# Optimization experiments

Measured on AMD Instinct MI355X. Metric: run time of the kernel, lower is better.

Reference implementation:

```python
import jax, jax.numpy as jnp
import numpy as np

NEG_BIG = -9e15

def mish(x):
    return x * jnp.tanh(jax.nn.softplus(x))

def setup_inputs() -> dict:
    key = jax.random.key(0)
    k1, k2, k3, k4 = jax.random.split(key, 4)
    N, Fin, Fout = 8192, 512, 256
    x = jax.random.normal(k1, (N, Fin), dtype=jnp.float32)
    adj = jax.random.randint(k2, (N, N), 0, 2, dtype=jnp.int32)
    # xavier-uniform-like params
    wlim = np.sqrt(6.0 / (Fin + Fout)).astype(np.float32)
    weight = jax.random.uniform(k3, (Fin, Fout), dtype=jnp.float32, minval=-wlim, maxval=wlim)
    alim = np.sqrt(6.0 / (2 * Fout + 1)).astype(np.float32)
    a = jax.random.uniform(k4, (2 * Fout, 1), dtype=jnp.float32, minval=-alim, maxval=alim)
    return {"x": x, "adj": adj, "weight": weight, "a": a}

def reference(x, adj, weight, a):
    Fout = weight.shape[1]
    h = x @ weight                      # [N, Fout]
    # e[i,j] = mish(h_i . a1 + h_j . a2) -- avoids O(N^2 * 2F) a_input
    s_src = h @ a[:Fout, 0]             # [N]
    s_dst = h @ a[Fout:, 0]             # [N]
    e = mish(s_src[:, None] + s_dst[None, :])  # [N, N]
    logits = jnp.where(adj > 0, e, NEG_BIG)
    attention = jax.nn.softmax(logits, axis=1)  # dropout skipped (eval mode)
    h_prime = attention @ h             # [N, Fout]
    return mish(h_prime)
```

## Files before the change

kernel.cpp:

```cpp
#include <hip/hip_runtime.h>
#include <hip/hip_fp16.h>

#define NROWS 8192
#define FIN   512
#define FOUT  256

using f16   = _Float16;
using f16x8 = __attribute__((ext_vector_type(8))) f16;
using f16x4 = __attribute__((ext_vector_type(4))) f16;
using f32x4 = __attribute__((ext_vector_type(4))) float;
using i32x4 = __attribute__((ext_vector_type(4))) int;

#define MFMA16(a, b, c) __builtin_amdgcn_mfma_f32_16x16x32_f16((a), (b), (c), 0, 0, 0)

__device__ __forceinline__ float mish_f(float x) {
  float t = __expf(x);
  float u = t * (t + 2.0f);
  return x * (u / (u + 2.0f));
}

__device__ __forceinline__ float dot4(float4 p, float4 q) {
  return p.x * q.x + p.y * q.y + p.z * q.z + p.w * q.w;
}

__global__ __launch_bounds__(256) void k0_prep_w(
    const float* __restrict__ wgt, const float* __restrict__ a,
    f16* __restrict__ wB_hi, f16* __restrict__ wB_lo,
    float* __restrict__ wa1, float* __restrict__ wa2) {
  int k = blockIdx.x * 256 + threadIdx.x;
  if (k >= FIN) return;
  int kt = k >> 5, g2 = (k >> 3) & 3, e = k & 7;
  float acc1 = 0.f, acc2 = 0.f;
  for (int f = 0; f < FOUT; ++f) {
    float v = wgt[(size_t)k * FOUT + f];
    acc1 += v * a[f];
    acc2 += v * a[FOUT + f];
    f16 h = (f16)v;
    size_t base = (((size_t)(kt * 16 + (f >> 4)) * 64) + g2 * 16 + (f & 15)) * 8 + e;
    wB_hi[base] = h;
    wB_lo[base] = (f16)(v - (float)h);
  }
  wa1[k] = acc1;
  wa2[k] = acc2;
}

__global__ __launch_bounds__(256) void k2_scores(
    const float* __restrict__ x, const float* __restrict__ wa1,
    const float* __restrict__ wa2, float* __restrict__ s_src,
    float* __restrict__ s_dst, unsigned int* __restrict__ maxd_enc) {
  int wv = threadIdx.x >> 6, lane = threadIdx.x & 63;
  int row = blockIdx.x * 4 + wv;
  const float4* xr = (const float4*)(x + (size_t)row * FIN);
  float4 x0 = xr[lane * 2], x1 = xr[lane * 2 + 1];
  const float4* w1 = (const float4*)wa1;
  const float4* w2 = (const float4*)wa2;
  float p1 = dot4(x0, w1[lane * 2]) + dot4(x1, w1[lane * 2 + 1]);
  float p2 = dot4(x0, w2[lane * 2]) + dot4(x1, w2[lane * 2 + 1]);
  for (int off = 32; off > 0; off >>= 1) {
    p1 += __shfl_down(p1, off);
    p2 += __shfl_down(p2, off);
  }
  if (lane == 0) {
    s_src[row] = p1;
    s_dst[row] = p2;
    unsigned b = __float_as_uint(p2);
    unsigned enc = (b & 0x80000000u) ? ~b : (b | 0x80000000u);
    atomicMax(maxd_enc, enc);
  }
}

__global__ __launch_bounds__(256) void k1_gemm_h(
    const float* __restrict__ x, const f16* __restrict__ wB_hi,
    const f16* __restrict__ wB_lo, f16* __restrict__ hB_hi,
    f16* __restrict__ hB_lo) {
  __shared__ float xs[64][36];
  int mt = blockIdx.x >> 1, ns = blockIdx.x & 1;
  int m0 = mt * 64;
  int tid = threadIdx.x;
  int w = tid >> 6, lane = tid & 63;
  int g = lane >> 4, lr = lane & 15;

  f32x4 acc[4][2] = {};

  for (int kk = 0; kk < FIN; kk += 32) {
    {
      int r = tid >> 3;
      int c = (tid & 7) * 4;
      *(float4*)(&xs[r][c])      = *(const float4*)(x + (size_t)(m0 + r) * FIN + kk + c);
      *(float4*)(&xs[r + 32][c]) = *(const float4*)(x + (size_t)(m0 + r + 32) * FIN + kk + c);
    }
    __syncthreads();
    int kt = kk >> 5;
    f16x8 bh[2], bl[2];
#pragma unroll
    for (int ct = 0; ct < 2; ++ct) {
      int ft = ns * 8 + w * 2 + ct;
      size_t slot = ((size_t)(kt * 16 + ft) * 64 + lane) * 8;
      bh[ct] = *(const f16x8*)(wB_hi + slot);
      bl[ct] = *(const f16x8*)(wB_lo + slot);
    }
#pragma unroll
    for (int rt = 0; rt < 4; ++rt) {
      const float* ap = &xs[rt * 16 + lr][g * 8];
      f16x8 ah, al;
#pragma unroll
      for (int e = 0; e < 8; ++e) {
        float v = ap[e];
        f16 h = (f16)v;
        ah[e] = h;
        al[e] = (f16)(v - (float)h);
      }
#pragma unroll
      for (int ct = 0; ct < 2; ++ct) {
        acc[rt][ct] = MFMA16(ah, bh[ct], acc[rt][ct]);
        acc[rt][ct] = MFMA16(ah, bl[ct], acc[rt][ct]);
        acc[rt][ct] = MFMA16(al, bh[ct], acc[rt][ct]);
      }
    }
    __syncthreads();
  }

#pragma unroll
  for (int rt = 0; rt < 4; ++rt) {
    int jg0 = m0 + rt * 16 + g * 4;
    int jt = jg0 >> 5, g2 = (jg0 >> 3) & 3, e0 = jg0 & 7;
#pragma unroll
    for (int ct = 0; ct < 2; ++ct) {
      int f = ns * 128 + w * 32 + ct * 16 + lr;
      size_t base = (((size_t)(jt * 16 + (f >> 4)) * 64) + g2 * 16 + (f & 15)) * 8 + e0;
      f16x4 hv, lv;
#pragma unroll
      for (int rg = 0; rg < 4; ++rg) {
        float v = acc[rt][ct][rg];
        f16 h = (f16)v;
        hv[rg] = h;
        lv[rg] = (f16)(v - (float)h);
      }
      *(f16x4*)(hB_hi + base) = hv;
      *(f16x4*)(hB_lo + base) = lv;
    }
  }
}

__global__ __launch_bounds__(256) void k3_attn(
    const int* __restrict__ adj, const f16* __restrict__ hB_hi,
    const f16* __restrict__ hB_lo, const float* __restrict__ s_src,
    const float* __restrict__ s_dst, const unsigned int* __restrict__ maxd_enc,
    float* __restrict__ num, float* __restrict__ Zbuf) {
  __shared__ float sd_lds[1024];
  __shared__ f16x8 pbuf[2][4][64];

  int it = blockIdx.x >> 3, jc = blockIdx.x & 7;
  int i0 = it * 64;
  int j0 = jc * 1024;
  int tid = threadIdx.x;
  int w = tid >> 6, lane = tid & 63;
  int g = lane >> 4, lr = lane & 15;

  *(float4*)(&sd_lds[tid * 4]) = *(const float4*)(s_dst + j0 + tid * 4);

  unsigned enc = *maxd_enc;
  float maxd = (enc & 0x80000000u) ? __uint_as_float(enc & 0x7fffffffu)
                                   : __uint_as_float(~enc);
  int ip = i0 + w * 16 + lr;
  float s_i = s_src[ip];
  float m_i = fmaxf(0.f, s_i + maxd);
  const int* adjrow = adj + (size_t)ip * NROWS + j0 + g * 8;

  __syncthreads();

  f32x4 acc[4][4] = {};
  f32x4 accz = {};
  f16x8 ones;
#pragma unroll
  for (int e = 0; e < 8; ++e) ones[e] = (f16)1.0f;

  i32x4 adjA = *(const i32x4*)(adjrow);
  i32x4 adjB = *(const i32x4*)(adjrow + 4);

  for (int st = 0; st < 32; ++st) {
    i32x4 nadjA = adjA, nadjB = adjB;
    if (st < 31) {
      nadjA = *(const i32x4*)(adjrow + (st + 1) * 32);
      nadjB = *(const i32x4*)(adjrow + (st + 1) * 32 + 4);
    }
    float4 sd0 = *(const float4*)(&sd_lds[st * 32 + g * 8]);
    float4 sd1 = *(const float4*)(&sd_lds[st * 32 + g * 8 + 4]);
    float sdv[8] = {sd0.x, sd0.y, sd0.z, sd0.w, sd1.x, sd1.y, sd1.z, sd1.w};

    f16x8 pa;
#pragma unroll
    for (int e = 0; e < 8; ++e) {
      float s = s_i + sdv[e];
      float t = __expf(s);
      float u = t * (t + 2.0f);
      float sc = s * (u / (u + 2.0f));
      float p = __expf(sc - m_i);
      int av = (e < 4) ? adjA[e] : adjB[e - 4];
      pa[e] = (av != 0) ? (f16)p : (f16)0.0f;
    }
    pbuf[st & 1][w][lane] = pa;
    accz = MFMA16(pa, ones, accz);
    __syncthreads();

    f16x8 afr[4];
#pragma unroll
    for (int rt = 0; rt < 4; ++rt) afr[rt] = pbuf[st & 1][rt][lane];

    int jt = jc * 32 + st;
#pragma unroll
    for (int ct = 0; ct < 4; ++ct) {
      int ft = w * 4 + ct;
      size_t slot = ((size_t)(jt * 16 + ft) * 64 + lane) * 8;
      f16x8 bhv = *(const f16x8*)(hB_hi + slot);
      f16x8 blv = *(const f16x8*)(hB_lo + slot);
#pragma unroll
      for (int rt = 0; rt < 4; ++rt) {
        acc[rt][ct] = MFMA16(afr[rt], bhv, acc[rt][ct]);
        acc[rt][ct] = MFMA16(afr[rt], blv, acc[rt][ct]);
      }
    }
    adjA = nadjA;
    adjB = nadjB;
  }

#pragma unroll
  for (int rt = 0; rt < 4; ++rt) {
    int ib = i0 + rt * 16 + g * 4;
#pragma unroll
    for (int ct = 0; ct < 4; ++ct) {
      int f = w * 64 + ct * 16 + lr;
#pragma unroll
      for (int rg = 0; rg < 4; ++rg)
        atomicAdd(&num[(size_t)(ib + rg) * FOUT + f], acc[rt][ct][rg]);
    }
  }
  if (lr == 0) {
    int ib = i0 + w * 16 + g * 4;
#pragma unroll
    for (int rg = 0; rg < 4; ++rg)
      atomicAdd(&Zbuf[ib + rg], accz[rg]);
  }
}

__global__ __launch_bounds__(256) void k4_final(float* __restrict__ out,
                                                const float* __restrict__ Zbuf) {
  int idx = blockIdx.x * 256 + threadIdx.x;
  int row = idx >> 6;
  float rz = 1.0f / Zbuf[row];
  float4 v = *(float4*)(out + (size_t)idx * 4);
  v.x = mish_f(v.x * rz);
  v.y = mish_f(v.y * rz);
  v.z = mish_f(v.z * rz);
  v.w = mish_f(v.w * rz);
  *(float4*)(out + (size_t)idx * 4) = v;
}

extern "C" void kernel_launch(void* const* d_in, const int* in_sizes, int n_in,
                              void* d_out, int out_size, void* d_ws, size_t ws_size,
                              hipStream_t stream) {
  const float* x   = (const float*)d_in[0];
  const int*   adj = (const int*)d_in[1];
  const float* wgt = (const float*)d_in[2];
  const float* a   = (const float*)d_in[3];
  float* out = (float*)d_out;

  char* ws = (char*)d_ws;
  f16* hB_hi = (f16*)ws;
  f16* hB_lo = (f16*)(ws + (4u << 20));
  f16* wB_hi = (f16*)(ws + (8u << 20));
  f16* wB_lo = (f16*)(ws + (8u << 20) + (256u << 10));
  float* wa1   = (float*)(ws + (8u << 20) + (512u << 10));
  float* wa2   = wa1 + FIN;
  float* s_src = wa2 + FIN;
  float* s_dst = s_src + NROWS;
  float* Zbuf  = s_dst + NROWS;
  unsigned int* maxd = (unsigned int*)(Zbuf + NROWS);

  hipMemsetAsync(d_out, 0, (size_t)out_size * sizeof(float), stream);
  hipMemsetAsync(Zbuf, 0, NROWS * sizeof(float) + sizeof(unsigned int), stream);

  k0_prep_w<<<2, 256, 0, stream>>>(wgt, a, wB_hi, wB_lo, wa1, wa2);
  k2_scores<<<NROWS / 4, 256, 0, stream>>>(x, wa1, wa2, s_src, s_dst, maxd);
  k1_gemm_h<<<(NROWS / 64) * 2, 256, 0, stream>>>(x, wB_hi, wB_lo, hB_hi, hB_lo);
  k3_attn<<<(NROWS / 64) * 8, 256, 0, stream>>>(adj, hB_hi, hB_lo, s_src, s_dst,
                                                maxd, out, Zbuf);
  k4_final<<<out_size / 4 / 256, 256, 0, stream>>>(out, Zbuf);
}
```

Measured before the change: 681.0 us.

## Fuse softmax normalization into attention kernel, drop atomics, parallelize weight prep

The attention kernel now gives each 512-thread block 16 full rows across all 8192 columns. Row sums and numerators therefore finish inside the block, and the final divide plus mish is applied directly when writing the output. This removes the output and Zbuf memsets, the float atomics and the separate finalize kernel. The weight-prep kernel also changes from 2 blocks of serial loops to one block per input row with a wave-shuffle reduction. In exchange, every block streams the whole fp16 h operand with a 16-row MFMA tile, which raises L2 and global traffic for h, and the grid is smaller.

```diff
diff --git a/kernel.cpp b/kernel.cpp
--- a/kernel.cpp
+++ b/kernel.cpp
@@ -23,25 +23,31 @@
   return p.x * q.x + p.y * q.y + p.z * q.z + p.w * q.w;
 }
 
-__global__ __launch_bounds__(256) void k0_prep_w(
+__global__ __launch_bounds__(256) void k0_prep(
     const float* __restrict__ wgt, const float* __restrict__ a,
     f16* __restrict__ wB_hi, f16* __restrict__ wB_lo,
     float* __restrict__ wa1, float* __restrict__ wa2) {
-  int k = blockIdx.x * 256 + threadIdx.x;
-  if (k >= FIN) return;
+  int k = blockIdx.x, f = threadIdx.x;
+  float v = wgt[(size_t)k * FOUT + f];
   int kt = k >> 5, g2 = (k >> 3) & 3, e = k & 7;
-  float acc1 = 0.f, acc2 = 0.f;
-  for (int f = 0; f < FOUT; ++f) {
-    float v = wgt[(size_t)k * FOUT + f];
-    acc1 += v * a[f];
-    acc2 += v * a[FOUT + f];
-    f16 h = (f16)v;
-    size_t base = (((size_t)(kt * 16 + (f >> 4)) * 64) + g2 * 16 + (f & 15)) * 8 + e;
-    wB_hi[base] = h;
-    wB_lo[base] = (f16)(v - (float)h);
-  }
-  wa1[k] = acc1;
-  wa2[k] = acc2;
+  size_t base = (((size_t)(kt * 16 + (f >> 4)) * 64) + g2 * 16 + (f & 15)) * 8 + e;
+  f16 h = (f16)v;
+  wB_hi[base] = h;
+  wB_lo[base] = (f16)(v - (float)h);
+
+  float p1 = v * a[f], p2 = v * a[FOUT + f];
+  for (int off = 32; off > 0; off >>= 1) {
+    p1 += __shfl_down(p1, off);
+    p2 += __shfl_down(p2, off);
+  }
+  __shared__ float red[8];
+  int w = threadIdx.x >> 6, lane = threadIdx.x & 63;
+  if (lane == 0) { red[w] = p1; red[4 + w] = p2; }
+  __syncthreads();
+  if (threadIdx.x == 0) {
+    wa1[k] = red[0] + red[1] + red[2] + red[3];
+    wa2[k] = red[4] + red[5] + red[6] + red[7];
+  }
 }
 
 __global__ __launch_bounds__(256) void k2_scores(
@@ -142,118 +148,104 @@
   }
 }
 
-__global__ __launch_bounds__(256) void k3_attn(
+__global__ __launch_bounds__(512) void k3_attn(
     const int* __restrict__ adj, const f16* __restrict__ hB_hi,
     const f16* __restrict__ hB_lo, const float* __restrict__ s_src,
     const float* __restrict__ s_dst, const unsigned int* __restrict__ maxd_enc,
-    float* __restrict__ num, float* __restrict__ Zbuf) {
-  __shared__ float sd_lds[1024];
-  __shared__ f16x8 pbuf[2][4][64];
-
-  int it = blockIdx.x >> 3, jc = blockIdx.x & 7;
-  int i0 = it * 64;
-  int j0 = jc * 1024;
+    float* __restrict__ out) {
+  __shared__ float sd[NROWS];
+  __shared__ __align__(16) f16 pb[2][4][64][8];
+  __shared__ float zl[16];
+
   int tid = threadIdx.x;
   int w = tid >> 6, lane = tid & 63;
-  int g = lane >> 4, lr = lane & 15;
-
-  *(float4*)(&sd_lds[tid * 4]) = *(const float4*)(s_dst + j0 + tid * 4);
+  int i0 = blockIdx.x * 16;
+
+#pragma unroll
+  for (int u = 0; u < 4; ++u)
+    *(float4*)(&sd[(u * 512 + tid) * 4]) =
+        *(const float4*)(s_dst + (u * 512 + tid) * 4);
 
   unsigned enc = *maxd_enc;
   float maxd = (enc & 0x80000000u) ? __uint_as_float(enc & 0x7fffffffu)
                                    : __uint_as_float(~enc);
-  int ip = i0 + w * 16 + lr;
-  float s_i = s_src[ip];
+  int r = tid >> 5;
+  int q = tid & 31;
+  int row = i0 + r;
+  float s_i = s_src[row];
   float m_i = fmaxf(0.f, s_i + maxd);
-  const int* adjrow = adj + (size_t)ip * NROWS + j0 + g * 8;
-
-  __syncthreads();
-
-  f32x4 acc[4][4] = {};
+  int sg = q >> 3;
+  int ee = (q & 7) * 4;
+  int lane_p = ((ee >> 3) << 4) + r;
+  int e0 = ee & 7;
+  const int* adjp = adj + (size_t)row * NROWS + q * 4;
+
+  __syncthreads();
+
+  f32x4 acc[2] = {};
   f32x4 accz = {};
   f16x8 ones;
 #pragma unroll
   for (int e = 0; e < 8; ++e) ones[e] = (f16)1.0f;
 
-  i32x4 adjA = *(const i32x4*)(adjrow);
-  i32x4 adjB = *(const i32x4*)(adjrow + 4);
-
-  for (int st = 0; st < 32; ++st) {
-    i32x4 nadjA = adjA, nadjB = adjB;
-    if (st < 31) {
-      nadjA = *(const i32x4*)(adjrow + (st + 1) * 32);
-      nadjB = *(const i32x4*)(adjrow + (st + 1) * 32 + 4);
-    }
-    float4 sd0 = *(const float4*)(&sd_lds[st * 32 + g * 8]);
-    float4 sd1 = *(const float4*)(&sd_lds[st * 32 + g * 8 + 4]);
-    float sdv[8] = {sd0.x, sd0.y, sd0.z, sd0.w, sd1.x, sd1.y, sd1.z, sd1.w};
-
-    f16x8 pa;
-#pragma unroll
-    for (int e = 0; e < 8; ++e) {
-      float s = s_i + sdv[e];
+  i32x4 av0 = *(const i32x4*)(adjp);
+  i32x4 av1 = *(const i32x4*)(adjp + 128);
+
+  for (int g = 0; g < 64; ++g) {
+    i32x4 ac = (g & 1) ? av1 : av0;
+    if (g + 2 < 64) {
+      if (g & 1) av1 = *(const i32x4*)(adjp + (size_t)(g + 2) * 128);
+      else       av0 = *(const i32x4*)(adjp + (size_t)(g + 2) * 128);
+    }
+    float4 sdv = *(const float4*)(&sd[g * 128 + q * 4]);
+    float sa[4] = {sdv.x, sdv.y, sdv.z, sdv.w};
+    f16x4 pv;
+#pragma unroll
+    for (int c = 0; c < 4; ++c) {
+      float s = s_i + sa[c];
       float t = __expf(s);
       float u = t * (t + 2.0f);
-      float sc = s * (u / (u + 2.0f));
+      float sc = s * __fdividef(u, u + 2.0f);
       float p = __expf(sc - m_i);
-      int av = (e < 4) ? adjA[e] : adjB[e - 4];
-      pa[e] = (av != 0) ? (f16)p : (f16)0.0f;
-    }
-    pbuf[st & 1][w][lane] = pa;
-    accz = MFMA16(pa, ones, accz);
+      pv[c] = (ac[c] != 0) ? (f16)p : (f16)0.0f;
+    }
+    *(f16x4*)(&pb[g & 1][sg][lane_p][e0]) = pv;
     __syncthreads();
 
-    f16x8 afr[4];
-#pragma unroll
-    for (int rt = 0; rt < 4; ++rt) afr[rt] = pbuf[st & 1][rt][lane];
-
-    int jt = jc * 32 + st;
-#pragma unroll
-    for (int ct = 0; ct < 4; ++ct) {
-      int ft = w * 4 + ct;
-      size_t slot = ((size_t)(jt * 16 + ft) * 64 + lane) * 8;
-      f16x8 bhv = *(const f16x8*)(hB_hi + slot);
-      f16x8 blv = *(const f16x8*)(hB_lo + slot);
-#pragma unroll
-      for (int rt = 0; rt < 4; ++rt) {
-        acc[rt][ct] = MFMA16(afr[rt], bhv, acc[rt][ct]);
-        acc[rt][ct] = MFMA16(afr[rt], blv, acc[rt][ct]);
-      }
-    }
-    adjA = nadjA;
-    adjB = nadjB;
-  }
-
-#pragma unroll
-  for (int rt = 0; rt < 4; ++rt) {
-    int ib = i0 + rt * 16 + g * 4;
-#pragma unroll
-    for (int ct = 0; ct < 4; ++ct) {
-      int f = w * 64 + ct * 16 + lr;
-#pragma unroll
-      for (int rg = 0; rg < 4; ++rg)
-        atomicAdd(&num[(size_t)(ib + rg) * FOUT + f], acc[rt][ct][rg]);
-    }
-  }
-  if (lr == 0) {
-    int ib = i0 + w * 16 + g * 4;
-#pragma unroll
-    for (int rg = 0; rg < 4; ++rg)
-      atomicAdd(&Zbuf[ib + rg], accz[rg]);
-  }
-}
-
-__global__ __launch_bounds__(256) void k4_final(float* __restrict__ out,
-                                                const float* __restrict__ Zbuf) {
-  int idx = blockIdx.x * 256 + threadIdx.x;
-  int row = idx >> 6;
-  float rz = 1.0f / Zbuf[row];
-  float4 v = *(float4*)(out + (size_t)idx * 4);
-  v.x = mish_f(v.x * rz);
-  v.y = mish_f(v.y * rz);
-  v.z = mish_f(v.z * rz);
-  v.w = mish_f(v.w * rz);
-  *(float4*)(out + (size_t)idx * 4) = v;
+    int buf = g & 1;
+#pragma unroll
+    for (int s = 0; s < 4; ++s) {
+      f16x8 afr = *(const f16x8*)(pb[buf][s][lane]);
+      int jt = g * 4 + s;
+#pragma unroll
+      for (int ct = 0; ct < 2; ++ct) {
+        int ft = w * 2 + ct;
+        size_t slot = ((size_t)(jt * 16 + ft) * 64 + lane) * 8;
+        f16x8 bhv = *(const f16x8*)(hB_hi + slot);
+        f16x8 blv = *(const f16x8*)(hB_lo + slot);
+        acc[ct] = MFMA16(afr, bhv, acc[ct]);
+        acc[ct] = MFMA16(afr, blv, acc[ct]);
+      }
+      if (w == 0) accz = MFMA16(afr, ones, accz);
+    }
+  }
+
+  __syncthreads();
+  if (w == 0 && (lane & 15) == 0) {
+#pragma unroll
+    for (int rg = 0; rg < 4; ++rg) zl[(lane >> 4) * 4 + rg] = accz[rg];
+  }
+  __syncthreads();
+
+#pragma unroll
+  for (int ct = 0; ct < 2; ++ct) {
+#pragma unroll
+    for (int rg = 0; rg < 4; ++rg) {
+      int rr = (lane >> 4) * 4 + rg;
+      float v = mish_f(acc[ct][rg] / zl[rr]);
+      out[(size_t)(i0 + rr) * FOUT + w * 32 + ct * 16 + (lane & 15)] = v;
+    }
+  }
 }
 
 extern "C" void kernel_launch(void* const* d_in, const int* in_sizes, int n_in,
@@ -274,16 +266,13 @@
   float* wa2   = wa1 + FIN;
   float* s_src = wa2 + FIN;
   float* s_dst = s_src + NROWS;
-  float* Zbuf  = s_dst + NROWS;
-  unsigned int* maxd = (unsigned int*)(Zbuf + NROWS);
-
-  hipMemsetAsync(d_out, 0, (size_t)out_size * sizeof(float), stream);
-  hipMemsetAsync(Zbuf, 0, NROWS * sizeof(float) + sizeof(unsigned int), stream);
-
-  k0_prep_w<<<2, 256, 0, stream>>>(wgt, a, wB_hi, wB_lo, wa1, wa2);
+  unsigned int* maxd = (unsigned int*)(s_dst + NROWS);
+
+  (void)hipMemsetAsync(maxd, 0, sizeof(unsigned int), stream);
+
+  k0_prep<<<FIN, 256, 0, stream>>>(wgt, a, wB_hi, wB_lo, wa1, wa2);
   k2_scores<<<NROWS / 4, 256, 0, stream>>>(x, wa1, wa2, s_src, s_dst, maxd);
   k1_gemm_h<<<(NROWS / 64) * 2, 256, 0, stream>>>(x, wB_hi, wB_lo, hB_hi, hB_lo);
-  k3_attn<<<(NROWS / 64) * 8, 256, 0, stream>>>(adj, hB_hi, hB_lo, s_src, s_dst,
-                                                maxd, out, Zbuf);
-  k4_final<<<out_size / 4 / 256, 256, 0, stream>>>(out, Zbuf);
-}
+  k3_attn<<<NROWS / 16, 512, 0, stream>>>(adj, hB_hi, hB_lo, s_src, s_dst,
+                                          maxd, out);
+}
```

After: 782.1 us. 1.15x slower.
